# Kernel tuning notes

Measured on AMD Instinct MI355X. Metric: run time of the kernel, lower is better.

The kernel has to match this reference:

```python
import jax, jax.numpy as jnp
import numpy as np

B, D, C, OUT = 16384, 784, 2048, 10

def setup_inputs() -> dict:
    key = jax.random.key(0)
    k1, k2, k3 = jax.random.split(key, 3)
    x = jax.random.normal(k1, (B, D), dtype=jnp.float32)
    centres = jax.random.normal(k2, (C, D), dtype=jnp.float32)
    log_sigmas = jnp.zeros((C,), dtype=jnp.float32)
    W = jax.random.normal(k3, (OUT, C), dtype=jnp.float32) * (1.0 / np.sqrt(C))
    b = jnp.zeros((OUT,), dtype=jnp.float32)
    return {"x": x, "centres": centres, "log_sigmas": log_sigmas, "W": W, "b": b}

def reference(x, centres, log_sigmas, W, b):
    # (B, C, D) broadcast tensor the torch code materializes; same math).
    x2 = jnp.sum(x * x, axis=-1, keepdims=True)          # (B, 1)
    c2 = jnp.sum(centres * centres, axis=-1)             # (C,)
    d2 = jnp.maximum(x2 + c2[None, :] - 2.0 * (x @ centres.T), 0.0)  # (B, C)
    distances = jnp.sqrt(d2) / jnp.exp(log_sigmas)[None, :]          # (B, C)
    phi = jnp.exp(-(distances * distances))              # gaussian basis
    return phi @ W.T + b                                  # (B, OUT)
```

## Files before the change

kernel.cpp:

```cpp
#include <hip/hip_runtime.h>


#define B_ROWS 16384
#define D_DIM  784
#define C_DIM  2048
#define NOUT   10
#define KPAD   832
#define BK     64

typedef __attribute__((ext_vector_type(8))) __bf16 bf16x8;
typedef __attribute__((ext_vector_type(4))) float  f32x4;
typedef __attribute__((ext_vector_type(4))) unsigned short ushort4v;

__device__ __forceinline__ unsigned short f2bf(float f) {
  union { float f; unsigned int u; } v; v.f = f;
  unsigned int u = v.u;
  return (unsigned short)((u + 0x7fffu + ((u >> 16) & 1u)) >> 16);
}

__device__ __forceinline__ void async16(const unsigned short* g, unsigned short* l) {
  __builtin_amdgcn_global_load_lds((const __attribute__((address_space(1))) void*)g,
                                   (__attribute__((address_space(3))) void*)l,
                                   16, 0, 0);
}

__global__ __launch_bounds__(256) void prep_rows(const float* __restrict__ src,
                                                 unsigned short* __restrict__ dst,
                                                 float* __restrict__ sq) {
  const int row  = blockIdx.x * 4 + (threadIdx.x >> 6);
  const int lane = threadIdx.x & 63;
  const float* s = src + (size_t)row * D_DIM;
  unsigned short* d = dst + (size_t)row * KPAD;
  float acc = 0.f;
#pragma unroll
  for (int c = 0; c < 4; ++c) {
    const int ch = lane + c * 64;
    if (ch < 196) {
      const float4 v = ((const float4*)s)[ch];
      ushort4v o; o.x = f2bf(v.x); o.y = f2bf(v.y); o.z = f2bf(v.z); o.w = f2bf(v.w);
      *(ushort4v*)(d + ch * 4) = o;
      acc += v.x * v.x + v.y * v.y + v.z * v.z + v.w * v.w;
    } else if (ch < 208) {
      ushort4v z = {0, 0, 0, 0};
      *(ushort4v*)(d + ch * 4) = z;
    }
  }
#pragma unroll
  for (int off = 32; off > 0; off >>= 1) acc += __shfl_down(acc, off);
  if (lane == 0) sq[row] = acc;
}

__global__ __launch_bounds__(256) void prep_misc(const float* __restrict__ ls,
                                                 const float* __restrict__ W,
                                                 const float* __restrict__ bias,
                                                 float* __restrict__ scale,
                                                 unsigned short* __restrict__ wb,
                                                 float* __restrict__ out) {
  const int i = blockIdx.x * 256 + threadIdx.x;
  if (i < B_ROWS * NOUT) out[i] = bias[i % NOUT];
  const int j = i - B_ROWS * NOUT;
  if (j >= 0 && j < 16 * C_DIM)
    wb[j] = ((j >> 11) < NOUT) ? f2bf(W[(j >> 11) * C_DIM + (j & 2047)]) : (unsigned short)0;
  const int k = j - 16 * C_DIM;
  if (k >= 0 && k < C_DIM) scale[k] = __expf(-2.f * ls[k]);
}

__global__ __launch_bounds__(256, 4) void rbf_main(
    const unsigned short* __restrict__ xb, const unsigned short* __restrict__ cb,
    const unsigned short* __restrict__ wb,
    const float* __restrict__ x2, const float* __restrict__ c2,
    const float* __restrict__ scale, float* __restrict__ out) {
  __shared__ char smem[34816];
  unsigned short* As = (unsigned short*)smem;
  unsigned short* Bs = (unsigned short*)(smem + 16384);
  unsigned short* Ph = (unsigned short*)smem;
  __shared__ float x2s[128], c2s[128], scs[128];

  const int tid  = threadIdx.x;
  const int w    = tid >> 6;
  const int lane = tid & 63;
  const int q    = lane >> 4;
  const int l16  = lane & 15;
  const int brow = blockIdx.x * 128;
  const int bcol = blockIdx.y * 128;

  if (tid < 128) x2s[tid] = x2[brow + tid];
  else { c2s[tid - 128] = c2[bcol + tid - 128]; scs[tid - 128] = scale[bcol + tid - 128]; }

  const int srow = tid >> 3;
  const int skc  = (tid & 7) ^ (srow & 7);
  const unsigned short* gA = xb + (size_t)(brow + srow) * KPAD + skc * 8;
  const unsigned short* gB = cb + (size_t)(bcol + srow) * KPAD + skc * 8;
  unsigned short* lA = &As[w * 512];
  unsigned short* lB = &Bs[w * 512];

  const int wr = (w >> 1) * 64;
  const int wc = (w & 1) * 64;
  const int swz = l16 & 7;

  f32x4 acc[4][4] = {};

  for (int k0 = 0; k0 < KPAD; k0 += BK) {
#pragma unroll
    for (int r = 0; r < 4; ++r) {
      async16(gA + (size_t)r * 32 * KPAD + k0, lA + r * 2048);
      async16(gB + (size_t)r * 32 * KPAD + k0, lB + r * 2048);
    }
    __syncthreads();
#pragma unroll
    for (int ks = 0; ks < 2; ++ks) {
      bf16x8 af[4], bfr[4];
#pragma unroll
      for (int i = 0; i < 4; ++i)
        af[i] = *(const bf16x8*)&As[(wr + i * 16 + l16) * 64 + (((ks * 4 + q) ^ swz) << 3)];
#pragma unroll
      for (int j = 0; j < 4; ++j)
        bfr[j] = *(const bf16x8*)&Bs[(wc + j * 16 + l16) * 64 + (((ks * 4 + q) ^ swz) << 3)];
#pragma unroll
      for (int i = 0; i < 4; ++i)
#pragma unroll
        for (int j = 0; j < 4; ++j)
          acc[i][j] = __builtin_amdgcn_mfma_f32_16x16x32_bf16(af[i], bfr[j], acc[i][j], 0, 0, 0);
    }
    __syncthreads();
  }

#pragma unroll
  for (int i = 0; i < 4; ++i) {
#pragma unroll
    for (int j = 0; j < 4; ++j) {
      const int cl = wc + j * 16 + l16;
      const float c2v = c2s[cl];
      const float sc = scs[cl];
#pragma unroll
      for (int r = 0; r < 4; ++r) {
        const int rl = wr + i * 16 + q * 4 + r;
        float d2 = x2s[rl] + c2v - 2.f * acc[i][j][r];
        d2 = fmaxf(d2, 0.f);
        const float phi = __expf(-d2 * sc);
        Ph[rl * 136 + cl] = f2bf(phi);
      }
    }
  }
  __syncthreads();

  f32x4 oacc[2] = {};
#pragma unroll
  for (int kk = 0; kk < 4; ++kk) {
    const bf16x8 bw = *(const bf16x8*)&wb[(size_t)l16 * C_DIM + bcol + kk * 32 + q * 8];
#pragma unroll
    for (int mi = 0; mi < 2; ++mi) {
      const bf16x8 ap = *(const bf16x8*)&Ph[(w * 32 + mi * 16 + l16) * 136 + kk * 32 + q * 8];
      oacc[mi] = __builtin_amdgcn_mfma_f32_16x16x32_bf16(ap, bw, oacc[mi], 0, 0, 0);
    }
  }
  if (l16 < NOUT) {
#pragma unroll
    for (int mi = 0; mi < 2; ++mi)
#pragma unroll
      for (int r = 0; r < 4; ++r) {
        const int grow = brow + w * 32 + mi * 16 + q * 4 + r;
        atomicAdd(&out[grow * NOUT + l16], oacc[mi][r]);
      }
  }
}

extern "C" void kernel_launch(void* const* d_in, const int* in_sizes, int n_in,
                              void* d_out, int out_size, void* d_ws, size_t ws_size,
                              hipStream_t stream) {
  const float* x    = (const float*)d_in[0];
  const float* cen  = (const float*)d_in[1];
  const float* ls   = (const float*)d_in[2];
  const float* W    = (const float*)d_in[3];
  const float* bias = (const float*)d_in[4];
  float* out = (float*)d_out;

  unsigned char* ws = (unsigned char*)d_ws;
  unsigned short* xb  = (unsigned short*)(ws);
  unsigned short* cbf = (unsigned short*)(ws + 27262976);
  unsigned short* wb  = (unsigned short*)(ws + 30670848);
  float* x2 = (float*)(ws + 30736384);
  float* c2 = (float*)(ws + 30801920);
  float* sc = (float*)(ws + 30810112);

  prep_rows<<<B_ROWS / 4, 256, 0, stream>>>(x, xb, x2);
  prep_rows<<<C_DIM / 4, 256, 0, stream>>>(cen, cbf, c2);
  prep_misc<<<(B_ROWS * NOUT + 16 * C_DIM + C_DIM + 255) / 256, 256, 0, stream>>>(
      ls, W, bias, sc, wb, out);
  rbf_main<<<dim3(B_ROWS / 128, C_DIM / 128), 256, 0, stream>>>(xb, cbf, wb, x2, c2, sc, out);
}
```

Before: 166.0 us.

## Enlarge GEMM tile to 256x256 with double-buffered async LDS pipeline and fused prep

Merges the three preprocessing kernels into one launch. The main kernel moves to 256x256 tiles with 512 threads, and each wave now computes a 128x64 sub-tile. The K loop double-buffers the A/B tiles, issuing the next tile's async global-to-LDS loads between MFMA phases with explicit vmcnt waits and setprio around the MFMAs. This aims to hide load latency, raise data reuse and cut launch overhead. The cost is about 135KB of LDS per block, which limits occupancy, and fewer blocks in the grid (64x8).

```diff
diff --git a/kernel.cpp b/kernel.cpp
--- a/kernel.cpp
+++ b/kernel.cpp
@@ -7,6 +7,7 @@
 #define NOUT   10
 #define KPAD   832
 #define BK     64
+#define NT     13
 
 typedef __attribute__((ext_vector_type(8))) __bf16 bf16x8;
 typedef __attribute__((ext_vector_type(4))) float  f32x4;
@@ -24,11 +25,9 @@
                                    16, 0, 0);
 }
 
-__global__ __launch_bounds__(256) void prep_rows(const float* __restrict__ src,
-                                                 unsigned short* __restrict__ dst,
-                                                 float* __restrict__ sq) {
-  const int row  = blockIdx.x * 4 + (threadIdx.x >> 6);
-  const int lane = threadIdx.x & 63;
+__device__ __forceinline__ void conv_row(const float* __restrict__ src,
+                                         unsigned short* __restrict__ dst,
+                                         float* __restrict__ sq, int row, int lane) {
   const float* s = src + (size_t)row * D_DIM;
   unsigned short* d = dst + (size_t)row * KPAD;
   float acc = 0.f;
@@ -50,83 +49,140 @@
   if (lane == 0) sq[row] = acc;
 }
 
-__global__ __launch_bounds__(256) void prep_misc(const float* __restrict__ ls,
-                                                 const float* __restrict__ W,
-                                                 const float* __restrict__ bias,
-                                                 float* __restrict__ scale,
-                                                 unsigned short* __restrict__ wb,
-                                                 float* __restrict__ out) {
-  const int i = blockIdx.x * 256 + threadIdx.x;
-  if (i < B_ROWS * NOUT) out[i] = bias[i % NOUT];
-  const int j = i - B_ROWS * NOUT;
-  if (j >= 0 && j < 16 * C_DIM)
-    wb[j] = ((j >> 11) < NOUT) ? f2bf(W[(j >> 11) * C_DIM + (j & 2047)]) : (unsigned short)0;
-  const int k = j - 16 * C_DIM;
-  if (k >= 0 && k < C_DIM) scale[k] = __expf(-2.f * ls[k]);
-}
-
-__global__ __launch_bounds__(256, 4) void rbf_main(
+__global__ __launch_bounds__(256) void prep_all(
+    const float* __restrict__ x, const float* __restrict__ cen,
+    const float* __restrict__ ls, const float* __restrict__ W,
+    const float* __restrict__ bias,
+    unsigned short* __restrict__ xb, unsigned short* __restrict__ cb,
+    unsigned short* __restrict__ wb,
+    float* __restrict__ x2, float* __restrict__ c2, float* __restrict__ sc,
+    float* __restrict__ out) {
+  const int bx = blockIdx.x;
+  if (bx < B_ROWS / 4) {
+    conv_row(x, xb, x2, bx * 4 + (threadIdx.x >> 6), threadIdx.x & 63);
+  } else if (bx < B_ROWS / 4 + C_DIM / 4) {
+    conv_row(cen, cb, c2, (bx - B_ROWS / 4) * 4 + (threadIdx.x >> 6), threadIdx.x & 63);
+  } else {
+    const int i = (bx - (B_ROWS / 4 + C_DIM / 4)) * 256 + threadIdx.x;
+    if (i < B_ROWS * NOUT) out[i] = bias[i % NOUT];
+    const int j = i - B_ROWS * NOUT;
+    if (j >= 0 && j < 16 * C_DIM)
+      wb[j] = ((j >> 11) < NOUT) ? f2bf(W[(j >> 11) * C_DIM + (j & 2047)]) : (unsigned short)0;
+    const int k = j - 16 * C_DIM;
+    if (k >= 0 && k < C_DIM) sc[k] = __expf(-2.f * ls[k]);
+  }
+}
+
+__global__ __launch_bounds__(512, 2) void rbf_main(
     const unsigned short* __restrict__ xb, const unsigned short* __restrict__ cb,
     const unsigned short* __restrict__ wb,
     const float* __restrict__ x2, const float* __restrict__ c2,
     const float* __restrict__ scale, float* __restrict__ out) {
-  __shared__ char smem[34816];
-  unsigned short* As = (unsigned short*)smem;
-  unsigned short* Bs = (unsigned short*)(smem + 16384);
+  __shared__ __align__(16) char smem[138240];
   unsigned short* Ph = (unsigned short*)smem;
-  __shared__ float x2s[128], c2s[128], scs[128];
+  float* x2s = (float*)(smem + 135168);
+  float* c2s = (float*)(smem + 136192);
+  float* scs = (float*)(smem + 137216);
 
   const int tid  = threadIdx.x;
   const int w    = tid >> 6;
   const int lane = tid & 63;
   const int q    = lane >> 4;
   const int l16  = lane & 15;
-  const int brow = blockIdx.x * 128;
-  const int bcol = blockIdx.y * 128;
-
-  if (tid < 128) x2s[tid] = x2[brow + tid];
-  else { c2s[tid - 128] = c2[bcol + tid - 128]; scs[tid - 128] = scale[bcol + tid - 128]; }
+  const int swz  = l16 & 7;
+  const int brow = blockIdx.x * 256;
+  const int bcol = blockIdx.y * 256;
+  const int wr   = (w >> 2) * 128;
+  const int wc   = (w & 3) * 64;
+
+  if (tid < 256) { c2s[tid] = c2[bcol + tid]; scs[tid] = scale[bcol + tid]; }
+  else           { x2s[tid - 256] = x2[brow + tid - 256]; }
 
   const int srow = tid >> 3;
   const int skc  = (tid & 7) ^ (srow & 7);
   const unsigned short* gA = xb + (size_t)(brow + srow) * KPAD + skc * 8;
   const unsigned short* gB = cb + (size_t)(bcol + srow) * KPAD + skc * 8;
-  unsigned short* lA = &As[w * 512];
-  unsigned short* lB = &Bs[w * 512];
-
-  const int wr = (w >> 1) * 64;
-  const int wc = (w & 1) * 64;
-  const int swz = l16 & 7;
-
-  f32x4 acc[4][4] = {};
-
-  for (int k0 = 0; k0 < KPAD; k0 += BK) {
-#pragma unroll
-    for (int r = 0; r < 4; ++r) {
-      async16(gA + (size_t)r * 32 * KPAD + k0, lA + r * 2048);
-      async16(gB + (size_t)r * 32 * KPAD + k0, lB + r * 2048);
-    }
-    __syncthreads();
-#pragma unroll
-    for (int ks = 0; ks < 2; ++ks) {
-      bf16x8 af[4], bfr[4];
-#pragma unroll
-      for (int i = 0; i < 4; ++i)
-        af[i] = *(const bf16x8*)&As[(wr + i * 16 + l16) * 64 + (((ks * 4 + q) ^ swz) << 3)];
-#pragma unroll
-      for (int j = 0; j < 4; ++j)
-        bfr[j] = *(const bf16x8*)&Bs[(wc + j * 16 + l16) * 64 + (((ks * 4 + q) ^ swz) << 3)];
-#pragma unroll
-      for (int i = 0; i < 4; ++i)
-#pragma unroll
-        for (int j = 0; j < 4; ++j)
-          acc[i][j] = __builtin_amdgcn_mfma_f32_16x16x32_bf16(af[i], bfr[j], acc[i][j], 0, 0, 0);
-    }
-    __syncthreads();
-  }
-
-#pragma unroll
-  for (int i = 0; i < 4; ++i) {
+  const int ldst = w * 512;
+
+#define STG_A(P, K0, R) async16(gA + (size_t)(R) * 64 * KPAD + (K0), (P) + (R) * 4096 + ldst)
+#define STG_B(P, K0, R) async16(gB + (size_t)(R) * 64 * KPAD + (K0), (P) + (R) * 4096 + ldst)
+
+  {
+    unsigned short* A0 = (unsigned short*)smem;
+    unsigned short* B0 = (unsigned short*)(smem + 32768);
+    STG_B(B0, 0, 0); STG_B(B0, 0, 1); STG_B(B0, 0, 2); STG_B(B0, 0, 3);
+    STG_A(A0, 0, 0); STG_A(A0, 0, 2); STG_A(A0, 0, 1); STG_A(A0, 0, 3);
+  }
+  asm volatile("s_waitcnt vmcnt(2) lgkmcnt(0)" ::: "memory");
+  __builtin_amdgcn_s_barrier();
+
+  f32x4 acc[8][4] = {};
+
+#define LD_A(IH, KS)                                                        \
+  _Pragma("unroll")                                                         \
+  for (int ii = 0; ii < 4; ++ii)                                            \
+    af[ii] = *(const bf16x8*)&As[(wr + (IH) * 64 + ii * 16 + l16) * 64 +    \
+                                 ((((KS) * 4 + q) ^ swz) << 3)];
+#define LD_B(KS)                                                            \
+  _Pragma("unroll")                                                         \
+  for (int j = 0; j < 4; ++j)                                               \
+    bfr[j] = *(const bf16x8*)&Bs[(wc + j * 16 + l16) * 64 +                 \
+                                 ((((KS) * 4 + q) ^ swz) << 3)];
+#define MFMA16(IOFF)                                                        \
+  __builtin_amdgcn_s_setprio(1);                                            \
+  _Pragma("unroll")                                                         \
+  for (int ii = 0; ii < 4; ++ii)                                            \
+    _Pragma("unroll")                                                       \
+    for (int j = 0; j < 4; ++j)                                             \
+      acc[(IOFF) + ii][j] = __builtin_amdgcn_mfma_f32_16x16x32_bf16(        \
+          af[ii], bfr[j], acc[(IOFF) + ii][j], 0, 0, 0);                    \
+  __builtin_amdgcn_s_setprio(0);
+
+  for (int t = 0; t < NT; ++t) {
+    char* base_r = smem + (t & 1) * 65536;
+    char* base_s = smem + ((t + 1) & 1) * 65536;
+    unsigned short* As  = (unsigned short*)base_r;
+    unsigned short* Bs  = (unsigned short*)(base_r + 32768);
+    unsigned short* Asn = (unsigned short*)base_s;
+    unsigned short* Bsn = (unsigned short*)(base_s + 32768);
+    const int kn = (t + 1) * BK;
+    const bool st = (t < NT - 1);
+    bf16x8 af[4], bfr[4];
+
+    LD_A(0, 0)
+    LD_B(0)
+    if (st) { STG_B(Bsn, kn, 0); STG_B(Bsn, kn, 1); }
+    __builtin_amdgcn_s_barrier();
+    MFMA16(0)
+    if (st) asm volatile("s_waitcnt vmcnt(2)" ::: "memory");
+    else    asm volatile("s_waitcnt vmcnt(0)" ::: "memory");
+    __builtin_amdgcn_s_barrier();
+
+    LD_A(1, 0)
+    if (st) { STG_B(Bsn, kn, 2); STG_B(Bsn, kn, 3); }
+    __builtin_amdgcn_s_barrier();
+    MFMA16(4)
+    __builtin_amdgcn_s_barrier();
+
+    LD_A(0, 1)
+    LD_B(1)
+    if (st) { STG_A(Asn, kn, 0); STG_A(Asn, kn, 2); }
+    __builtin_amdgcn_s_barrier();
+    MFMA16(0)
+    __builtin_amdgcn_s_barrier();
+
+    LD_A(1, 1)
+    if (st) { STG_A(Asn, kn, 1); STG_A(Asn, kn, 3); }
+    __builtin_amdgcn_s_barrier();
+    MFMA16(4)
+    if (st) asm volatile("s_waitcnt vmcnt(2)" ::: "memory");
+    __builtin_amdgcn_s_barrier();
+  }
+
+  __syncthreads();
+
+#pragma unroll
+  for (int i = 0; i < 8; ++i) {
 #pragma unroll
     for (int j = 0; j < 4; ++j) {
       const int cl = wc + j * 16 + l16;
@@ -135,10 +191,8 @@
 #pragma unroll
       for (int r = 0; r < 4; ++r) {
         const int rl = wr + i * 16 + q * 4 + r;
-        float d2 = x2s[rl] + c2v - 2.f * acc[i][j][r];
-        d2 = fmaxf(d2, 0.f);
-        const float phi = __expf(-d2 * sc);
-        Ph[rl * 136 + cl] = f2bf(phi);
+        float d2 = fmaxf(x2s[rl] + c2v - 2.f * acc[i][j][r], 0.f);
+        Ph[rl * 264 + cl] = f2bf(__expf(-d2 * sc));
       }
     }
   }
@@ -146,11 +200,11 @@
 
   f32x4 oacc[2] = {};
 #pragma unroll
-  for (int kk = 0; kk < 4; ++kk) {
+  for (int kk = 0; kk < 8; ++kk) {
     const bf16x8 bw = *(const bf16x8*)&wb[(size_t)l16 * C_DIM + bcol + kk * 32 + q * 8];
 #pragma unroll
     for (int mi = 0; mi < 2; ++mi) {
-      const bf16x8 ap = *(const bf16x8*)&Ph[(w * 32 + mi * 16 + l16) * 136 + kk * 32 + q * 8];
+      const bf16x8 ap = *(const bf16x8*)&Ph[(w * 32 + mi * 16 + l16) * 264 + kk * 32 + q * 8];
       oacc[mi] = __builtin_amdgcn_mfma_f32_16x16x32_bf16(ap, bw, oacc[mi], 0, 0, 0);
     }
   }
@@ -163,6 +217,11 @@
         atomicAdd(&out[grow * NOUT + l16], oacc[mi][r]);
       }
   }
+#undef STG_A
+#undef STG_B
+#undef LD_A
+#undef LD_B
+#undef MFMA16
 }
 
 extern "C" void kernel_launch(void* const* d_in, const int* in_sizes, int n_in,
@@ -183,9 +242,8 @@
   float* c2 = (float*)(ws + 30801920);
   float* sc = (float*)(ws + 30810112);
 
-  prep_rows<<<B_ROWS / 4, 256, 0, stream>>>(x, xb, x2);
-  prep_rows<<<C_DIM / 4, 256, 0, stream>>>(cen, cbf, c2);
-  prep_misc<<<(B_ROWS * NOUT + 16 * C_DIM + C_DIM + 255) / 256, 256, 0, stream>>>(
-      ls, W, bias, sc, wb, out);
-  rbf_main<<<dim3(B_ROWS / 128, C_DIM / 128), 256, 0, stream>>>(xb, cbf, wb, x2, c2, sc, out);
-}
+  const int prep_blocks = B_ROWS / 4 + C_DIM / 4 +
+                          (B_ROWS * NOUT + 16 * C_DIM + C_DIM + 255) / 256;
+  prep_all<<<prep_blocks, 256, 0, stream>>>(x, cen, ls, W, bias, xb, cbf, wb, x2, c2, sc, out);
+  rbf_main<<<dim3(B_ROWS / 256, C_DIM / 256), 512, 0, stream>>>(xb, cbf, wb, x2, c2, sc, out);
+}
```

Result: faster. 157.5 us (-5.1%).
